# Kernel tuning notes

Measured on AMD Instinct MI355X. Metric: run time of the kernel, lower is better.

The kernel has to match this reference:

```python
import jax, jax.numpy as jnp
import numpy as np

N_HEAD = 16

def _rope_cache(dim, T):
    # matches precompute_rope_cache: angles = outer(pos, 1/theta^(2i/dim))
    pos = jnp.arange(T, dtype=jnp.float32)
    freq = 1.0 / (10000.0 ** (jnp.arange(0, dim, 2, dtype=jnp.float32) / dim))
    ang = pos[:, None] * freq[None, :]  # (T, dim//2)
    return jnp.cos(ang), jnp.sin(ang)

def _apply_rope(x, cos, sin):
    # x: (B, H, T, hs). Faithful to the (nonstandard, roll-based) torch apply_rope,
    # including the reassignment of x_rot before it is used for x_pass.
    x_rot, x_pass = x[..., ::2], x[..., 1::2]
    c = cos[None, None]  # (1,1,T,hs//2)
    s = sin[None, None]
    new_rot = x_rot * c - jnp.roll(x_pass, 1, axis=-1) * s
    new_pass = x_pass * c + jnp.roll(new_rot, -1, axis=-1) * s
    return jnp.stack([new_rot, new_pass], axis=-1).reshape(x.shape)

def setup_inputs() -> dict:
    key = jax.random.key(0)
    k1, k2, k3 = jax.random.split(key, 3)
    B, T, C = 2, 2048, 1024
    x = jax.random.normal(k1, (B, T, C), dtype=jnp.float32)
    w_attn = jax.random.normal(k2, (3 * C, C), dtype=jnp.float32) * 0.02
    w_proj = jax.random.normal(k3, (C, C), dtype=jnp.float32) * 0.02
    return {"x": x, "w_attn": w_attn, "w_proj": w_proj}

def reference(x, w_attn, w_proj):
    B, T, C = x.shape
    H = N_HEAD
    hs = C // H
    qkv = jnp.einsum('btc,dc->btd', x, w_attn)  # fused QKV projection (no bias)
    q, k, v = jnp.split(qkv, 3, axis=-1)
    def heads(t):
        return t.reshape(B, T, H, hs).transpose(0, 2, 1, 3)  # (B,H,T,hs)
    q, k, v = heads(q), heads(k), heads(v)
    cos, sin = _rope_cache(hs, T)
    q = _apply_rope(q, cos, sin)
    k = _apply_rope(k, cos, sin)
    scores = jnp.einsum('bhqd,bhkd->bhqk', q, k) / jnp.sqrt(jnp.float32(hs))
    causal = jnp.tril(jnp.ones((T, T), dtype=bool))
    scores = jnp.where(causal[None, None], scores, -jnp.inf)
    att = jax.nn.softmax(scores, axis=-1)
    y = jnp.einsum('bhqk,bhkd->bhqd', att, v)
    y = y.transpose(0, 2, 1, 3).reshape(B, T, C)
    return jnp.einsum('btc,dc->btd', y, w_proj)
```

## Files before the change

kernel.cpp:

```cpp
#include <hip/hip_runtime.h>

#define T_SEQ 2048
#define NHEAD 16
#define HS 64

typedef __bf16 bf16x8 __attribute__((ext_vector_type(8)));
typedef float f32x4 __attribute__((ext_vector_type(4)));

__device__ __forceinline__ unsigned short f2bf(float f) {
  union { float f; unsigned int u; } v; v.f = f;
  return (unsigned short)((v.u + 0x7fffu + ((v.u >> 16) & 1u)) >> 16);
}
__device__ __forceinline__ float bf2f(unsigned short h) {
  union { unsigned int u; float f; } v; v.u = ((unsigned int)h) << 16;
  return v.f;
}
__device__ __forceinline__ bf16x8 ld_bf8(const unsigned short* p) {
  return *(const bf16x8*)p;
}
__device__ __forceinline__ void st_bf8(unsigned short* p, bf16x8 v) {
  *(bf16x8*)p = v;
}
__device__ __forceinline__ bf16x8 cvt8(float4 a, float4 b) {
  bf16x8 r;
  r[0] = (__bf16)a.x; r[1] = (__bf16)a.y; r[2] = (__bf16)a.z; r[3] = (__bf16)a.w;
  r[4] = (__bf16)b.x; r[5] = (__bf16)b.y; r[6] = (__bf16)b.z; r[7] = (__bf16)b.w;
  return r;
}

__global__ __launch_bounds__(256, 2) void gemm_bt(
    const void* __restrict__ Av, const void* __restrict__ Bv,
    float* __restrict__ Cout,
    unsigned short* __restrict__ qb, unsigned short* __restrict__ kb,
    unsigned short* __restrict__ vtb,
    int M, int N, int K, int af32, int bf32, int mode) {
  __shared__ unsigned short As[128 * 64];
  __shared__ unsigned short Bs[128 * 64];
  const int tid = threadIdx.x;
  const int wid = tid >> 6, lane = tid & 63;
  const int quad = lane >> 4, l16 = lane & 15;
  const int m0 = blockIdx.y * 128, n0 = blockIdx.x * 128;
  const int wm = (wid >> 1) * 64, wn = (wid & 1) * 64;
  const int row_in = tid >> 3;
  const int col_in = (tid & 7) * 8;
  const float* Agf = (const float*)Av + (size_t)(m0 + row_in) * K + col_in;
  const float* Bgf = (const float*)Bv + (size_t)(n0 + row_in) * K + col_in;
  const unsigned short* Agh = (const unsigned short*)Av + (size_t)(m0 + row_in) * K + col_in;
  const unsigned short* Bgh = (const unsigned short*)Bv + (size_t)(n0 + row_in) * K + col_in;
  f32x4 acc[4][4] = {};
  const int nkt = K >> 6;
  for (int kt = 0; kt < nkt; ++kt) {
    bf16x8 as8[4], bs8[4];
    if (af32) {
      #pragma unroll
      for (int j = 0; j < 4; ++j) {
        const float* p = Agf + (size_t)j * 32 * K + kt * 64;
        as8[j] = cvt8(*(const float4*)p, *(const float4*)(p + 4));
      }
    } else {
      #pragma unroll
      for (int j = 0; j < 4; ++j)
        as8[j] = ld_bf8(Agh + (size_t)j * 32 * K + kt * 64);
    }
    if (bf32) {
      #pragma unroll
      for (int j = 0; j < 4; ++j) {
        const float* p = Bgf + (size_t)j * 32 * K + kt * 64;
        bs8[j] = cvt8(*(const float4*)p, *(const float4*)(p + 4));
      }
    } else {
      #pragma unroll
      for (int j = 0; j < 4; ++j)
        bs8[j] = ld_bf8(Bgh + (size_t)j * 32 * K + kt * 64);
    }
    __syncthreads();
    #pragma unroll
    for (int j = 0; j < 4; ++j) {
      st_bf8(&As[(j * 32 + row_in) * 64 + col_in], as8[j]);
      st_bf8(&Bs[(j * 32 + row_in) * 64 + col_in], bs8[j]);
    }
    __syncthreads();
    #pragma unroll
    for (int ks = 0; ks < 2; ++ks) {
      bf16x8 af[4], bfr[4];
      #pragma unroll
      for (int mt = 0; mt < 4; ++mt)
        af[mt] = ld_bf8(&As[(wm + mt * 16 + l16) * 64 + ks * 32 + quad * 8]);
      #pragma unroll
      for (int nt = 0; nt < 4; ++nt)
        bfr[nt] = ld_bf8(&Bs[(wn + nt * 16 + l16) * 64 + ks * 32 + quad * 8]);
      #pragma unroll
      for (int mt = 0; mt < 4; ++mt)
        #pragma unroll
        for (int nt = 0; nt < 4; ++nt)
          acc[mt][nt] = __builtin_amdgcn_mfma_f32_16x16x32_bf16(af[mt], bfr[nt], acc[mt][nt], 0, 0, 0);
    }
  }
  #pragma unroll
  for (int mt = 0; mt < 4; ++mt) {
    #pragma unroll
    for (int nt = 0; nt < 4; ++nt) {
      const int n = n0 + wn + nt * 16 + l16;
      #pragma unroll
      for (int r = 0; r < 4; ++r) {
        const int m = m0 + wm + mt * 16 + quad * 4 + r;
        if (mode == 0) {
          Cout[(size_t)m * N + n] = acc[mt][nt][r];
        } else {
          const unsigned short val = f2bf(acc[mt][nt][r]);
          const int b = m >> 11, t = m & (T_SEQ - 1);
          const int which = n >> 10, c = n & 1023;
          const int h = c >> 6, d = c & 63;
          const int bh = b * NHEAD + h;
          if (which == 0)      qb[((size_t)bh * T_SEQ + t) * HS + d] = val;
          else if (which == 1) kb[((size_t)bh * T_SEQ + t) * HS + d] = val;
          else                 vtb[((size_t)bh * HS + d) * T_SEQ + t] = val;
        }
      }
    }
  }
}

__global__ __launch_bounds__(256, 1) void rope(unsigned short* __restrict__ qb,
                                               unsigned short* __restrict__ kb) {
  const int idx = blockIdx.x * 256 + threadIdx.x;
  unsigned short* buf = (idx < 65536 ? qb : kb) + (size_t)(idx & 65535) * HS;
  const int t = idx & (T_SEQ - 1);
  float x[64];
  #pragma unroll
  for (int j = 0; j < 64; ++j) x[j] = bf2f(buf[j]);
  __asm__ volatile("" ::: "memory");
  float c[32], s[32], er[32];
  #pragma unroll
  for (int i = 0; i < 32; ++i) {
    const float ang = (float)t * exp2f(-0.41524101186092029f * (float)i);
    c[i] = cosf(ang); s[i] = sinf(ang);
  }
  #pragma unroll
  for (int i = 0; i < 32; ++i)
    er[i] = x[2 * i] * c[i] - x[(2 * i + 63) & 63] * s[i];
  #pragma unroll
  for (int i = 0; i < 32; ++i) {
    const float ep = x[2 * i + 1] * c[i] + er[(i + 1) & 31] * s[i];
    buf[2 * i]     = f2bf(er[i]);
    buf[2 * i + 1] = f2bf(ep);
  }
}

__global__ __launch_bounds__(64) void attn(
    const unsigned short* __restrict__ qb, const unsigned short* __restrict__ kb,
    const unsigned short* __restrict__ vt, unsigned short* __restrict__ yb) {
  __shared__ __bf16 Pl[16][72];
  const int u = blockIdx.x;
  const int qi = 127 - (u >> 5);
  const int bh = u & 31;
  const int q0 = qi * 16;
  const int lane = threadIdx.x & 63;
  const int quad = lane >> 4, l16 = lane & 15;

  const unsigned short* qptr = qb + ((size_t)bh * T_SEQ + q0 + l16) * HS;
  const bf16x8 aq0 = ld_bf8(qptr + quad * 8);
  const bf16x8 aq1 = ld_bf8(qptr + 32 + quad * 8);
  f32x4 O[4] = {};
  float m_i[4], l_i[4], alpha[4];
  #pragma unroll
  for (int r = 0; r < 4; ++r) { m_i[r] = -1e30f; l_i[r] = 0.f; }

  const unsigned short* kbase = kb + (size_t)bh * T_SEQ * HS;
  const unsigned short* vbase = vt + (size_t)bh * HS * T_SEQ;
  const int kend = q0 + 15;

  for (int k0 = 0; k0 <= kend; k0 += 64) {
    bf16x8 bk[4][2];
    #pragma unroll
    for (int t = 0; t < 4; ++t) {
      const unsigned short* kp = kbase + (size_t)(k0 + t * 16 + l16) * HS;
      bk[t][0] = ld_bf8(kp + quad * 8);
      bk[t][1] = ld_bf8(kp + 32 + quad * 8);
    }
    f32x4 S[4] = {};
    #pragma unroll
    for (int t = 0; t < 4; ++t) {
      S[t] = __builtin_amdgcn_mfma_f32_16x16x32_bf16(aq0, bk[t][0], S[t], 0, 0, 0);
      S[t] = __builtin_amdgcn_mfma_f32_16x16x32_bf16(aq1, bk[t][1], S[t], 0, 0, 0);
    }
    bf16x8 vb[2][4];
    #pragma unroll
    for (int c = 0; c < 2; ++c)
      #pragma unroll
      for (int vg = 0; vg < 4; ++vg)
        vb[c][vg] = ld_bf8(vbase + (size_t)(vg * 16 + l16) * T_SEQ + k0 + c * 32 + quad * 8);
    #pragma unroll
    for (int r = 0; r < 4; ++r) {
      const int row = q0 + quad * 4 + r;
      float s[4];
      #pragma unroll
      for (int t = 0; t < 4; ++t)
        s[t] = (k0 + t * 16 + l16 <= row) ? S[t][r] * 0.125f : -1e30f;
      float tm = fmaxf(fmaxf(s[0], s[1]), fmaxf(s[2], s[3]));
      #pragma unroll
      for (int off = 1; off < 16; off <<= 1) tm = fmaxf(tm, __shfl_xor(tm, off, 64));
      const float mnew = fmaxf(m_i[r], tm);
      alpha[r] = __expf(m_i[r] - mnew);
      unsigned short h[4];
      float rs = 0.f;
      #pragma unroll
      for (int t = 0; t < 4; ++t) {
        h[t] = f2bf(__expf(s[t] - mnew));
        rs += bf2f(h[t]);
      }
      #pragma unroll
      for (int off = 1; off < 16; off <<= 1) rs += __shfl_xor(rs, off, 64);
      l_i[r] = l_i[r] * alpha[r] + rs;
      m_i[r] = mnew;
      #pragma unroll
      for (int t = 0; t < 4; ++t)
        Pl[quad * 4 + r][t * 16 + l16] = __builtin_bit_cast(__bf16, h[t]);
    }
    #pragma unroll
    for (int vg = 0; vg < 4; ++vg)
      #pragma unroll
      for (int r = 0; r < 4; ++r) O[vg][r] *= alpha[r];
    #pragma unroll
    for (int c = 0; c < 2; ++c) {
      const bf16x8 pa = *(const bf16x8*)&Pl[l16][c * 32 + quad * 8];
      #pragma unroll
      for (int vg = 0; vg < 4; ++vg)
        O[vg] = __builtin_amdgcn_mfma_f32_16x16x32_bf16(pa, vb[c][vg], O[vg], 0, 0, 0);
    }
  }
  const int b = bh >> 4, h = bh & 15;
  #pragma unroll
  for (int r = 0; r < 4; ++r) {
    const float inv = 1.0f / fmaxf(l_i[r], 1e-30f);
    const int row = q0 + quad * 4 + r;
    #pragma unroll
    for (int vg = 0; vg < 4; ++vg)
      yb[((size_t)b * T_SEQ + row) * 1024 + h * HS + vg * 16 + l16] = f2bf(O[vg][r] * inv);
  }
}

extern "C" void kernel_launch(void* const* d_in, const int* in_sizes, int n_in,
                              void* d_out, int out_size, void* d_ws, size_t ws_size,
                              hipStream_t stream) {
  const float* x      = (const float*)d_in[0];
  const float* w_attn = (const float*)d_in[1];
  const float* w_proj = (const float*)d_in[2];
  float* out = (float*)d_out;
  unsigned short* qb = (unsigned short*)d_ws;
  unsigned short* kb = qb + (size_t)4194304;
  unsigned short* vt = kb + (size_t)4194304;
  unsigned short* yb = vt + (size_t)4194304;

  gemm_bt<<<dim3(24, 32), 256, 0, stream>>>(x, w_attn, nullptr, qb, kb, vt,
                                            4096, 3072, 1024, 1, 1, 1);
  rope<<<dim3(512), 256, 0, stream>>>(qb, kb);
  attn<<<dim3(4096), 64, 0, stream>>>(qb, kb, vt, yb);
  gemm_bt<<<dim3(8, 32), 256, 0, stream>>>(yb, w_proj, out, nullptr, nullptr, nullptr,
                                           4096, 1024, 1024, 0, 1, 0);
}
```

Baseline: 305.8 us.

## Keep attention probabilities in registers, fold scale into rope, pre-convert GEMM inputs to bf16

Attention now computes transposed scores (K as A operand) so each lane owns a query column. This lets the softmax probabilities feed a 16x16x16 bf16 MFMA directly from registers instead of going through shared memory. Causal masking applies only on the final diagonal block. The 1/sqrt(hs) scale is folded into the rope kernel for q. When the workspace is large enough, x and both weight matrices are converted to bf16 in separate kernels before the GEMMs, which adds extra launches and memory traffic.

```diff
diff --git a/kernel.cpp b/kernel.cpp
--- a/kernel.cpp
+++ b/kernel.cpp
@@ -6,6 +6,7 @@
 
 typedef __bf16 bf16x8 __attribute__((ext_vector_type(8)));
 typedef float f32x4 __attribute__((ext_vector_type(4)));
+typedef short short4v __attribute__((ext_vector_type(4)));
 
 __device__ __forceinline__ unsigned short f2bf(float f) {
   union { float f; unsigned int u; } v; v.f = f;
@@ -121,10 +122,23 @@
   }
 }
 
+__global__ __launch_bounds__(256) void cvtbuf(const float* __restrict__ src,
+                                              unsigned short* __restrict__ dst, int n) {
+  const int i = (blockIdx.x * 256 + threadIdx.x) * 4;
+  if (i < n) {
+    const float4 v = *(const float4*)(src + i);
+    ushort4 o;
+    o.x = f2bf(v.x); o.y = f2bf(v.y); o.z = f2bf(v.z); o.w = f2bf(v.w);
+    *(ushort4*)(dst + i) = o;
+  }
+}
+
 __global__ __launch_bounds__(256, 1) void rope(unsigned short* __restrict__ qb,
                                                unsigned short* __restrict__ kb) {
   const int idx = blockIdx.x * 256 + threadIdx.x;
-  unsigned short* buf = (idx < 65536 ? qb : kb) + (size_t)(idx & 65535) * HS;
+  const bool isq = idx < 65536;
+  const float qs = isq ? 0.125f : 1.0f;
+  unsigned short* buf = (isq ? qb : kb) + (size_t)(idx & 65535) * HS;
   const int t = idx & (T_SEQ - 1);
   float x[64];
   #pragma unroll
@@ -142,15 +156,14 @@
   #pragma unroll
   for (int i = 0; i < 32; ++i) {
     const float ep = x[2 * i + 1] * c[i] + er[(i + 1) & 31] * s[i];
-    buf[2 * i]     = f2bf(er[i]);
-    buf[2 * i + 1] = f2bf(ep);
-  }
-}
-
-__global__ __launch_bounds__(64) void attn(
+    buf[2 * i]     = f2bf(er[i] * qs);
+    buf[2 * i + 1] = f2bf(ep * qs);
+  }
+}
+
+__global__ __launch_bounds__(64, 4) void attn(
     const unsigned short* __restrict__ qb, const unsigned short* __restrict__ kb,
     const unsigned short* __restrict__ vt, unsigned short* __restrict__ yb) {
-  __shared__ __bf16 Pl[16][72];
   const int u = blockIdx.x;
   const int qi = 127 - (u >> 5);
   const int bh = u & 31;
@@ -159,84 +172,95 @@
   const int quad = lane >> 4, l16 = lane & 15;
 
   const unsigned short* qptr = qb + ((size_t)bh * T_SEQ + q0 + l16) * HS;
-  const bf16x8 aq0 = ld_bf8(qptr + quad * 8);
-  const bf16x8 aq1 = ld_bf8(qptr + 32 + quad * 8);
+  const bf16x8 bq0 = ld_bf8(qptr + quad * 8);
+  const bf16x8 bq1 = ld_bf8(qptr + 32 + quad * 8);
+
   f32x4 O[4] = {};
-  float m_i[4], l_i[4], alpha[4];
-  #pragma unroll
-  for (int r = 0; r < 4; ++r) { m_i[r] = -1e30f; l_i[r] = 0.f; }
+  float m_i = -1e30f, l_i = 0.f;
 
   const unsigned short* kbase = kb + (size_t)bh * T_SEQ * HS;
   const unsigned short* vbase = vt + (size_t)bh * HS * T_SEQ;
-  const int kend = q0 + 15;
-
-  for (int k0 = 0; k0 <= kend; k0 += 64) {
-    bf16x8 bk[4][2];
+  const int nfull = (q0 >= 63) ? (((q0 - 63) >> 6) + 1) : 0;
+
+  auto pass_body = [&](int k0, bool masked) {
+    bf16x8 ak[4][2];
     #pragma unroll
     for (int t = 0; t < 4; ++t) {
       const unsigned short* kp = kbase + (size_t)(k0 + t * 16 + l16) * HS;
-      bk[t][0] = ld_bf8(kp + quad * 8);
-      bk[t][1] = ld_bf8(kp + 32 + quad * 8);
-    }
+      ak[t][0] = ld_bf8(kp + quad * 8);
+      ak[t][1] = ld_bf8(kp + 32 + quad * 8);
+    }
+    short4v vf[4][4];
+    #pragma unroll
+    for (int t = 0; t < 4; ++t)
+      #pragma unroll
+      for (int dg = 0; dg < 4; ++dg)
+        vf[t][dg] = *(const short4v*)(vbase + (size_t)(dg * 16 + l16) * T_SEQ + k0 + t * 16 + quad * 4);
     f32x4 S[4] = {};
     #pragma unroll
     for (int t = 0; t < 4; ++t) {
-      S[t] = __builtin_amdgcn_mfma_f32_16x16x32_bf16(aq0, bk[t][0], S[t], 0, 0, 0);
-      S[t] = __builtin_amdgcn_mfma_f32_16x16x32_bf16(aq1, bk[t][1], S[t], 0, 0, 0);
-    }
-    bf16x8 vb[2][4];
-    #pragma unroll
-    for (int c = 0; c < 2; ++c)
-      #pragma unroll
-      for (int vg = 0; vg < 4; ++vg)
-        vb[c][vg] = ld_bf8(vbase + (size_t)(vg * 16 + l16) * T_SEQ + k0 + c * 32 + quad * 8);
-    #pragma unroll
-    for (int r = 0; r < 4; ++r) {
-      const int row = q0 + quad * 4 + r;
-      float s[4];
-      #pragma unroll
-      for (int t = 0; t < 4; ++t)
-        s[t] = (k0 + t * 16 + l16 <= row) ? S[t][r] * 0.125f : -1e30f;
-      float tm = fmaxf(fmaxf(s[0], s[1]), fmaxf(s[2], s[3]));
-      #pragma unroll
-      for (int off = 1; off < 16; off <<= 1) tm = fmaxf(tm, __shfl_xor(tm, off, 64));
-      const float mnew = fmaxf(m_i[r], tm);
-      alpha[r] = __expf(m_i[r] - mnew);
-      unsigned short h[4];
-      float rs = 0.f;
-      #pragma unroll
-      for (int t = 0; t < 4; ++t) {
-        h[t] = f2bf(__expf(s[t] - mnew));
-        rs += bf2f(h[t]);
+      S[t] = __builtin_amdgcn_mfma_f32_16x16x32_bf16(ak[t][0], bq0, S[t], 0, 0, 0);
+      S[t] = __builtin_amdgcn_mfma_f32_16x16x32_bf16(ak[t][1], bq1, S[t], 0, 0, 0);
+    }
+    float sv[16];
+    #pragma unroll
+    for (int t = 0; t < 4; ++t)
+      #pragma unroll
+      for (int r = 0; r < 4; ++r) {
+        float v = S[t][r];
+        if (masked) v = (k0 + t * 16 + quad * 4 + r <= q0 + l16) ? v : -1e30f;
+        sv[t * 4 + r] = v;
       }
-      #pragma unroll
-      for (int off = 1; off < 16; off <<= 1) rs += __shfl_xor(rs, off, 64);
-      l_i[r] = l_i[r] * alpha[r] + rs;
-      m_i[r] = mnew;
-      #pragma unroll
-      for (int t = 0; t < 4; ++t)
-        Pl[quad * 4 + r][t * 16 + l16] = __builtin_bit_cast(__bf16, h[t]);
-    }
-    #pragma unroll
-    for (int vg = 0; vg < 4; ++vg)
-      #pragma unroll
-      for (int r = 0; r < 4; ++r) O[vg][r] *= alpha[r];
-    #pragma unroll
-    for (int c = 0; c < 2; ++c) {
-      const bf16x8 pa = *(const bf16x8*)&Pl[l16][c * 32 + quad * 8];
-      #pragma unroll
-      for (int vg = 0; vg < 4; ++vg)
-        O[vg] = __builtin_amdgcn_mfma_f32_16x16x32_bf16(pa, vb[c][vg], O[vg], 0, 0, 0);
-    }
-  }
+    float tm = sv[0];
+    #pragma unroll
+    for (int i = 1; i < 16; ++i) tm = fmaxf(tm, sv[i]);
+    tm = fmaxf(tm, __shfl_xor(tm, 16, 64));
+    tm = fmaxf(tm, __shfl_xor(tm, 32, 64));
+    const float mnew = fmaxf(m_i, tm);
+    const float alpha = __expf(m_i - mnew);
+    float p[16], rs = 0.f;
+    #pragma unroll
+    for (int i = 0; i < 16; ++i) { p[i] = __expf(sv[i] - mnew); rs += p[i]; }
+    rs += __shfl_xor(rs, 16, 64);
+    rs += __shfl_xor(rs, 32, 64);
+    l_i = l_i * alpha + rs;
+    m_i = mnew;
+    short4v pa[4];
+    #pragma unroll
+    for (int t = 0; t < 4; ++t) {
+      short4v f;
+      f[0] = (short)f2bf(p[t * 4 + 0]); f[1] = (short)f2bf(p[t * 4 + 1]);
+      f[2] = (short)f2bf(p[t * 4 + 2]); f[3] = (short)f2bf(p[t * 4 + 3]);
+      pa[t] = f;
+    }
+    float aD[4];
+    #pragma unroll
+    for (int r = 0; r < 4; ++r) aD[r] = __shfl(alpha, quad * 4 + r, 64);
+    #pragma unroll
+    for (int dg = 0; dg < 4; ++dg)
+      #pragma unroll
+      for (int r = 0; r < 4; ++r) O[dg][r] *= aD[r];
+    #pragma unroll
+    for (int t = 0; t < 4; ++t)
+      #pragma unroll
+      for (int dg = 0; dg < 4; ++dg)
+        O[dg] = __builtin_amdgcn_mfma_f32_16x16x16bf16_1k(pa[t], vf[t][dg], O[dg], 0, 0, 0);
+  };
+
+  for (int k0 = 0; k0 < nfull * 64; k0 += 64) pass_body(k0, false);
+  pass_body(nfull * 64, true);
+
   const int b = bh >> 4, h = bh & 15;
+  float inv[4];
+  #pragma unroll
+  for (int r = 0; r < 4; ++r)
+    inv[r] = 1.0f / fmaxf(__shfl(l_i, quad * 4 + r, 64), 1e-30f);
   #pragma unroll
   for (int r = 0; r < 4; ++r) {
-    const float inv = 1.0f / fmaxf(l_i[r], 1e-30f);
     const int row = q0 + quad * 4 + r;
     #pragma unroll
-    for (int vg = 0; vg < 4; ++vg)
-      yb[((size_t)b * T_SEQ + row) * 1024 + h * HS + vg * 16 + l16] = f2bf(O[vg][r] * inv);
+    for (int dg = 0; dg < 4; ++dg)
+      yb[((size_t)b * T_SEQ + row) * 1024 + h * HS + dg * 16 + l16] = f2bf(O[dg][r] * inv[r]);
   }
 }
 
@@ -252,10 +276,25 @@
   unsigned short* vt = kb + (size_t)4194304;
   unsigned short* yb = vt + (size_t)4194304;
 
-  gemm_bt<<<dim3(24, 32), 256, 0, stream>>>(x, w_attn, nullptr, qb, kb, vt,
-                                            4096, 3072, 1024, 1, 1, 1);
-  rope<<<dim3(512), 256, 0, stream>>>(qb, kb);
-  attn<<<dim3(4096), 64, 0, stream>>>(qb, kb, vt, yb);
-  gemm_bt<<<dim3(8, 32), 256, 0, stream>>>(yb, w_proj, out, nullptr, nullptr, nullptr,
-                                           4096, 1024, 1024, 0, 1, 0);
-}
+  if (ws_size >= (size_t)50331648 + (size_t)2097152) {
+    unsigned short* xb  = yb + (size_t)4194304;
+    unsigned short* wab = xb + (size_t)4194304;
+    unsigned short* wpb = wab + (size_t)3145728;
+    cvtbuf<<<dim3(4096), 256, 0, stream>>>(x, xb, 4194304);
+    cvtbuf<<<dim3(3072), 256, 0, stream>>>(w_attn, wab, 3145728);
+    cvtbuf<<<dim3(1024), 256, 0, stream>>>(w_proj, wpb, 1048576);
+    gemm_bt<<<dim3(24, 32), 256, 0, stream>>>(xb, wab, nullptr, qb, kb, vt,
+                                              4096, 3072, 1024, 0, 0, 1);
+    rope<<<dim3(512), 256, 0, stream>>>(qb, kb);
+    attn<<<dim3(4096), 64, 0, stream>>>(qb, kb, vt, yb);
+    gemm_bt<<<dim3(8, 32), 256, 0, stream>>>(yb, wpb, out, nullptr, nullptr, nullptr,
+                                             4096, 1024, 1024, 0, 0, 0);
+  } else {
+    gemm_bt<<<dim3(24, 32), 256, 0, stream>>>(x, w_attn, nullptr, qb, kb, vt,
+                                              4096, 3072, 1024, 1, 1, 1);
+    rope<<<dim3(512), 256, 0, stream>>>(qb, kb);
+    attn<<<dim3(4096), 64, 0, stream>>>(qb, kb, vt, yb);
+    gemm_bt<<<dim3(8, 32), 256, 0, stream>>>(yb, w_proj, out, nullptr, nullptr, nullptr,
+                                             4096, 1024, 1024, 0, 1, 0);
+  }
+}
```

Result: slower. 353.6 us (+15.6%).
